# Performance work log

Measured on AMD Instinct MI355X. Metric: run time of the kernel, lower is better.

Reference implementation:

```python
import jax, jax.numpy as jnp
import numpy as np

B, T, C = 4, 2048, 2048
N_HEAD = 16
HEAD_DIM = C // N_HEAD


def setup_inputs() -> dict:
    key = jax.random.key(0)
    k1, k2, k3, k4, k5 = jax.random.split(key, 5)
    s = 1.0 / np.sqrt(C)
    return {
        "x": jax.random.normal(k1, (B, T, C), dtype=jnp.float32),
        "w_attn": jax.random.normal(k2, (C, 3 * C), dtype=jnp.float32) * s,
        "b_attn": jax.random.normal(k3, (3 * C,), dtype=jnp.float32) * 0.02,
        "w_proj": jax.random.normal(k4, (C, C), dtype=jnp.float32) * s,
        "b_proj": jax.random.normal(k5, (C,), dtype=jnp.float32) * 0.02,
    }


def reference(x, w_attn, b_attn, w_proj, b_proj):
    Bsz, Tlen, Cdim = x.shape
    # fused QKV projection
    qkv = x @ w_attn + b_attn  # [B,T,3C]
    q, k, v = jnp.split(qkv, 3, axis=-1)
    # [B,T,C] -> [B,H,T,D]
    def heads(t):
        return t.reshape(Bsz, Tlen, N_HEAD, HEAD_DIM).transpose(0, 2, 1, 3)
    q, k, v = heads(q), heads(k), heads(v)
    scale = 1.0 / np.sqrt(HEAD_DIM).astype(np.float32)
    att = jnp.einsum("bhqd,bhkd->bhqk", q, k) * scale  # [B,H,T,T]
    causal = jnp.tril(jnp.ones((Tlen, Tlen), dtype=bool))
    att = jnp.where(causal, att, -jnp.inf)
    att = jax.nn.softmax(att, axis=-1)
    y = jnp.einsum("bhqk,bhkd->bhqd", att, v)  # [B,H,T,D]
    y = y.transpose(0, 2, 1, 3).reshape(Bsz, Tlen, Cdim)
    return y @ w_proj + b_proj
```

## Files before the change

kernel.cpp:

```cpp
#include <hip/hip_runtime.h>

typedef __bf16 bf16x8 __attribute__((ext_vector_type(8)));
typedef __bf16 bf16x4 __attribute__((ext_vector_type(4)));
typedef float  f32x4  __attribute__((ext_vector_type(4)));
typedef float  f32x16 __attribute__((ext_vector_type(16)));
typedef unsigned u32x4 __attribute__((ext_vector_type(4)));

#define LOG2E 1.4426950408889634f

__device__ __forceinline__ void gload16(const void* g, void* l) {
  __builtin_amdgcn_global_load_lds((const __attribute__((address_space(1))) void*)g,
                                   (__attribute__((address_space(3))) void*)l, 16, 0, 0);
}

__device__ __forceinline__ unsigned pk(float lo, float hi) {
  unsigned short lu = __builtin_bit_cast(unsigned short, (__bf16)lo);
  unsigned short hu = __builtin_bit_cast(unsigned short, (__bf16)hi);
  return (unsigned)lu | ((unsigned)hu << 16);
}

__global__ __launch_bounds__(256) void cvt4(const float* __restrict__ in,
                                            __bf16* __restrict__ outp, int n4) {
  int i = blockIdx.x * blockDim.x + threadIdx.x;
  if (i < n4) {
    float4 v = ((const float4*)in)[i];
    bf16x4 o = { (__bf16)v.x, (__bf16)v.y, (__bf16)v.z, (__bf16)v.w };
    *(bf16x4*)(outp + (size_t)i * 4) = o;
  }
}

__global__ __launch_bounds__(256) void transcvt(const float* __restrict__ w,
                                                __bf16* __restrict__ wt,
                                                int K, int N) {
  __shared__ float tile[32][33];
  const int n0 = blockIdx.x * 32, k0 = blockIdx.y * 32;
  const int tx = threadIdx.x, ty = threadIdx.y;
#pragma unroll
  for (int i = 0; i < 4; ++i)
    tile[ty + i * 8][tx] = w[(size_t)(k0 + ty + i * 8) * N + n0 + tx];
  __syncthreads();
#pragma unroll
  for (int i = 0; i < 4; ++i)
    wt[(size_t)(n0 + ty + i * 8) * K + k0 + tx] = (__bf16)tile[tx][ty + i * 8];
}

template <int EPI, int NCOLS>
__global__ __launch_bounds__(512, 2)
void gemm_bt(const __bf16* __restrict__ A, const __bf16* __restrict__ Bt,
             const float* __restrict__ bias,
             __bf16* __restrict__ Qb, __bf16* __restrict__ Kb,
             __bf16* __restrict__ Vtb, float* __restrict__ Out) {
  constexpr int K = 2048;
  constexpr int NSTEP = K / 32;
  constexpr int NBX = NCOLS / 256;
  __shared__ __align__(16) __bf16 lds_[65536];
  __bf16* const As_ = lds_;
  __bf16* const Bs_ = lds_ + 32768;
  const int tid = threadIdx.x, lane = tid & 63, w = tid >> 6;
  const int wr = w >> 2, wc = w & 3;
  const int l15 = lane & 15, g = lane >> 4;

  const int nwg = (int)gridDim.x;
  const int flat = ((int)blockIdx.x & 7) * (nwg >> 3) + ((int)blockIdx.x >> 3);
  const int by = flat / NBX, bx = flat % NBX;

  const __bf16* Ab = A + (size_t)by * 256 * K;
  const __bf16* Bb = Bt + (size_t)bx * 256 * K;

  const int gsw = (((tid & 3) ^ ((tid >> 3) & 3)) * 8);
  const __bf16* srcA[2];
  const __bf16* srcB[2];
#pragma unroll
  for (int c = 0; c < 2; ++c) {
    const int idx = c * 512 + tid;
    const int row = idx >> 2;
    srcA[c] = Ab + (size_t)row * K + gsw;
    srcB[c] = Bb + (size_t)row * K + gsw;
  }
  const int ldst = tid * 8;

  const int csw = ((g ^ ((l15 >> 1) & 3)) * 8);

  f32x4 acc[8][4] = {};

#define ISSUE_A(jj) { const int s_ = ((jj) & 3) * 8192;                       \
    gload16(srcA[0] + (size_t)(jj) * 32, (void*)(As_ + s_ + ldst));           \
    gload16(srcA[1] + (size_t)(jj) * 32, (void*)(As_ + s_ + 4096 + ldst)); }
#define ISSUE_B(jj) { const int s_ = ((jj) & 3) * 8192;                       \
    gload16(srcB[0] + (size_t)(jj) * 32, (void*)(Bs_ + s_ + ldst));           \
    gload16(srcB[1] + (size_t)(jj) * 32, (void*)(Bs_ + s_ + 4096 + ldst)); }
#define VM8 asm volatile("s_waitcnt vmcnt(8)" ::: "memory")
#define VM4 asm volatile("s_waitcnt vmcnt(4)" ::: "memory")
#define VM0 asm volatile("s_waitcnt vmcnt(0)" ::: "memory")
#define VMN

#define KSTEP(j, ISS, VMW) {                                                  \
    const int rs = ((j) & 3) * 8192;                                          \
    bf16x8 av[8], bv[4];                                                      \
                           \
    _Pragma("unroll")                                                         \
    for (int i = 0; i < 4; ++i)                                               \
      bv[i] = *(const bf16x8*)(Bs_ + rs + (wc * 64 + i * 16 + l15) * 32 + csw); \
    _Pragma("unroll")                                                         \
    for (int i = 0; i < 4; ++i)                                               \
      av[i] = *(const bf16x8*)(As_ + rs + (wr * 128 + i * 16 + l15) * 32 + csw); \
    if (ISS) ISSUE_A((j) + 3);                                                \
    __builtin_amdgcn_s_barrier();                                             \
    __builtin_amdgcn_s_setprio(1);                                            \
    _Pragma("unroll")                                                         \
    for (int mi = 0; mi < 4; ++mi)                                            \
      _Pragma("unroll")                                                       \
      for (int ni = 0; ni < 4; ++ni)                                          \
        acc[mi][ni] = __builtin_amdgcn_mfma_f32_16x16x32_bf16(av[mi], bv[ni], \
                                                              acc[mi][ni], 0, 0, 0); \
    __builtin_amdgcn_s_setprio(0);                                            \
    __builtin_amdgcn_s_barrier();                                             \
            \
    _Pragma("unroll")                                                         \
    for (int i = 4; i < 8; ++i)                                               \
      av[i] = *(const bf16x8*)(As_ + rs + (wr * 128 + i * 16 + l15) * 32 + csw); \
    if (ISS) ISSUE_B((j) + 3);                                                \
    __builtin_amdgcn_s_barrier();                                             \
    __builtin_amdgcn_s_setprio(1);                                            \
    _Pragma("unroll")                                                         \
    for (int mi = 4; mi < 8; ++mi)                                            \
      _Pragma("unroll")                                                       \
      for (int ni = 0; ni < 4; ++ni)                                          \
        acc[mi][ni] = __builtin_amdgcn_mfma_f32_16x16x32_bf16(av[mi], bv[ni], \
                                                              acc[mi][ni], 0, 0, 0); \
    __builtin_amdgcn_s_setprio(0);                                            \
    VMW;                                                                      \
    __builtin_amdgcn_s_barrier();                                             \
  }

  ISSUE_A(0); ISSUE_B(0);
  ISSUE_A(1); ISSUE_B(1);
  ISSUE_A(2); ISSUE_B(2);
  VM8;
  __builtin_amdgcn_s_barrier();

  for (int j = 0; j < NSTEP - 3; ++j) KSTEP(j, true, VM8);
  KSTEP(NSTEP - 3, false, VM4);
  KSTEP(NSTEP - 2, false, VM0);
  KSTEP(NSTEP - 1, false, VMN);

#undef KSTEP
#undef ISSUE_A
#undef ISSUE_B

  const int r0 = by * 256 + wr * 128 + (g << 2);
  const int c0 = bx * 256 + wc * 64 + l15;
#pragma unroll
  for (int ni = 0; ni < 4; ++ni) {
    const int c = c0 + ni * 16;
    const float bvs = bias[c];
    if constexpr (EPI == 0) {
      const int sel = c >> 11, cc = c & 2047, h = cc >> 7, d = cc & 127;
#pragma unroll
      for (int mi = 0; mi < 8; ++mi) {
        const int r = r0 + mi * 16;
        const int bb = r >> 11, t = r & 2047;
        if (sel == 2) {
          bf16x4 pv;
#pragma unroll
          for (int j = 0; j < 4; ++j) pv[j] = (__bf16)(acc[mi][ni][j] + bvs);
          *(bf16x4*)(Vtb + ((size_t)(bb * 16 + h) * 128 + d) * 2048 + t) = pv;
        } else {
          __bf16* dst = (sel == 0 ? Qb : Kb) + ((size_t)(bb * 16 + h) * 2048 + t) * 128 + d;
          const float sc = (sel == 0) ? 0.08838834764831845f : 1.0f;
#pragma unroll
          for (int j = 0; j < 4; ++j)
            dst[(size_t)j * 128] = (__bf16)((acc[mi][ni][j] + bvs) * sc);
        }
      }
    } else {
#pragma unroll
      for (int mi = 0; mi < 8; ++mi) {
        const int r = r0 + mi * 16;
#pragma unroll
        for (int j = 0; j < 4; ++j)
          Out[(size_t)(r + j) * NCOLS + c] = acc[mi][ni][j] + bvs;
      }
    }
  }
}

__global__ __launch_bounds__(512, 2)
void attn_fwd(const __bf16* __restrict__ Qb, const __bf16* __restrict__ Kb,
              const __bf16* __restrict__ Vtb, __bf16* __restrict__ Yb) {
  __shared__ __align__(16) char lds[65536];
  const int tid = threadIdx.x;
  const int lane = tid & 63, w = tid >> 6;
  const int l31 = lane & 31, hi = lane >> 5;
  const int kx = (l31 & 7) << 4;

  const int G = (int)gridDim.x;
  for (int rr = 0;; ++rr) {
    const int pos = (rr & 1) ? (G - 1 - (int)blockIdx.x) : (int)blockIdx.x;
    const int item = rr * G + pos;
    if (item >= 512) break;
    const int qb = 7 - (item >> 6);
    const int bh = item & 63;
    const int bidx = bh >> 4, h = bh & 15;
    const int nt = (qb + 1) * 4;

    const __bf16* Qh = Qb + ((size_t)bh * 2048 + qb * 256) * 128;
    const __bf16* Kh = Kb + (size_t)bh * 2048 * 128;
    const __bf16* Vh = Vtb + (size_t)bh * 128 * 2048;

    bf16x8 qf[8];
    {
      const __bf16* qrow = Qh + (size_t)(w * 32 + l31) * 128 + hi * 8;
#pragma unroll
      for (int ds = 0; ds < 8; ++ds) qf[ds] = *(const bf16x8*)(qrow + ds * 16);
    }

    {
      uint4 kr[2], vr[2];
#pragma unroll
      for (int c = 0; c < 2; ++c) {
        const int idx = c * 512 + tid;
        kr[c] = *(const uint4*)(Kh + (size_t)(idx >> 4) * 128 + (idx & 15) * 8);
        vr[c] = *(const uint4*)(Vh + (size_t)(idx >> 3) * 2048 + (idx & 7) * 8);
      }
      __syncthreads();
      char* K0 = lds;
      char* V0 = lds + 16384;
#pragma unroll
      for (int c = 0; c < 2; ++c) {
        const int idx = c * 512 + tid;
        { const int row = idx >> 4, colB = (idx & 15) * 16;
          *(uint4*)(K0 + row * 256 + (colB ^ ((row & 7) << 4))) = kr[c]; }
        { const int row = idx >> 3, colB = (idx & 7) * 16;
          *(uint4*)(V0 + row * 128 + (colB ^ ((row & 7) << 4))) = vr[c]; }
      }
      __syncthreads();
    }

    f32x16 accO[4] = {};
    float mL = -3.0e38f, lsum = 0.f;
    const int qg  = qb * 256 + w * 32 + l31;
    const int qwb = qb * 256 + w * 32;

    for (int t = 0; t < nt; ++t) {
      const int kv0 = t * 64;
      char* Kc = lds + (t & 1) * 32768;
      char* Vc = Kc + 16384;
      const bool pf = (t + 1 < nt);
      uint4 kr[2], vr[2];
      if (pf) {
        const int kvn = kv0 + 64;
#pragma unroll
        for (int c = 0; c < 2; ++c) {
          const int idx = c * 512 + tid;
          kr[c] = *(const uint4*)(Kh + (size_t)(kvn + (idx >> 4)) * 128 + (idx & 15) * 8);
          vr[c] = *(const uint4*)(Vh + (size_t)(idx >> 3) * 2048 + kvn + (idx & 7) * 8);
        }
      }

      f32x16 s0 = {}, s1 = {};
      __builtin_amdgcn_s_setprio(1);
#pragma unroll
      for (int ds = 0; ds < 8; ++ds) {
        const int cb = (ds * 32 + hi * 16) ^ kx;
        bf16x8 k0 = *(const bf16x8*)(Kc + l31 * 256 + cb);
        bf16x8 k1 = *(const bf16x8*)(Kc + (32 + l31) * 256 + cb);
        s0 = __builtin_amdgcn_mfma_f32_32x32x16_bf16(k0, qf[ds], s0, 0, 0, 0);
        s1 = __builtin_amdgcn_mfma_f32_32x32x16_bf16(k1, qf[ds], s1, 0, 0, 0);
      }
      __builtin_amdgcn_s_setprio(0);

      f32x16 a0, a1;
#pragma unroll
      for (int r = 0; r < 16; ++r) { a0[r] = s0[r] * LOG2E; a1[r] = s1[r] * LOG2E; }
      if (kv0 + 63 > qwb) {
#pragma unroll
        for (int r = 0; r < 16; ++r) {
          const int kvr = kv0 + (r & 3) + 8 * (r >> 2) + 4 * hi;
          if (kvr > qg)      a0[r] = -1.0e38f;
          if (kvr + 32 > qg) a1[r] = -1.0e38f;
        }
      }

      float pm = a0[0];
#pragma unroll
      for (int r = 1; r < 16; ++r) pm = fmaxf(pm, a0[r]);
#pragma unroll
      for (int r = 0; r < 16; ++r) pm = fmaxf(pm, a1[r]);
      pm = fmaxf(pm, __shfl_xor(pm, 32, 64));

      if (!__all(pm - mL <= 11.5f)) {
        const float mn = fmaxf(mL, pm);
        const float corr = exp2f(mL - mn);
        mL = mn;
        lsum *= corr;
#pragma unroll
        for (int db = 0; db < 4; ++db)
#pragma unroll
          for (int r = 0; r < 16; ++r) accO[db][r] *= corr;
      }

      float p[32];
      float rs = 0.f;
#pragma unroll
      for (int r = 0; r < 16; ++r) { p[r] = exp2f(a0[r] - mL); rs += p[r]; }
#pragma unroll
      for (int r = 0; r < 16; ++r) { p[16 + r] = exp2f(a1[r] - mL); rs += p[16 + r]; }
      rs += __shfl_xor(rs, 32, 64);
      lsum += rs;

      bf16x8 pa[4];
#pragma unroll
      for (int f = 0; f < 2; ++f) {
        unsigned wv[8];
#pragma unroll
        for (int i = 0; i < 8; ++i)
          wv[i] = pk(p[f * 16 + 2 * i], p[f * 16 + 2 * i + 1]);
        const unsigned x0 = (unsigned)__shfl_xor((int)(hi ? wv[0] : wv[2]), 32, 64);
        const unsigned x1 = (unsigned)__shfl_xor((int)(hi ? wv[1] : wv[3]), 32, 64);
        const unsigned x2 = (unsigned)__shfl_xor((int)(hi ? wv[4] : wv[6]), 32, 64);
        const unsigned x3 = (unsigned)__shfl_xor((int)(hi ? wv[5] : wv[7]), 32, 64);
        u32x4 A, B;
        A[0] = hi ? x0 : wv[0];  A[1] = hi ? x1 : wv[1];
        A[2] = hi ? wv[2] : x0;  A[3] = hi ? wv[3] : x1;
        B[0] = hi ? x2 : wv[4];  B[1] = hi ? x3 : wv[5];
        B[2] = hi ? wv[6] : x2;  B[3] = hi ? wv[7] : x3;
        pa[f * 2 + 0] = __builtin_bit_cast(bf16x8, A);
        pa[f * 2 + 1] = __builtin_bit_cast(bf16x8, B);
      }

      __builtin_amdgcn_s_setprio(1);
#pragma unroll
      for (int ks = 0; ks < 4; ++ks) {
        const int cb = (ks * 32 + hi * 16) ^ kx;
#pragma unroll
        for (int db = 0; db < 4; ++db) {
          bf16x8 vf = *(const bf16x8*)(Vc + (db * 32 + l31) * 128 + cb);
          accO[db] = __builtin_amdgcn_mfma_f32_32x32x16_bf16(vf, pa[ks], accO[db], 0, 0, 0);
        }
      }
      __builtin_amdgcn_s_setprio(0);

      if (pf) {
        char* Kn = lds + ((t + 1) & 1) * 32768;
        char* Vn = Kn + 16384;
#pragma unroll
        for (int c = 0; c < 2; ++c) {
          const int idx = c * 512 + tid;
          { const int row = idx >> 4, colB = (idx & 15) * 16;
            *(uint4*)(Kn + row * 256 + (colB ^ ((row & 7) << 4))) = kr[c]; }
          { const int row = idx >> 3, colB = (idx & 7) * 16;
            *(uint4*)(Vn + row * 128 + (colB ^ ((row & 7) << 4))) = vr[c]; }
        }
      }
      __syncthreads();
    }

    const float rl = 1.0f / lsum;
    __bf16* Yw = Yb + ((size_t)bidx * 2048 + qg) * 2048 + h * 128;
#pragma unroll
    for (int db = 0; db < 4; ++db)
#pragma unroll
      for (int j = 0; j < 4; ++j) {
        bf16x4 o;
#pragma unroll
        for (int i = 0; i < 4; ++i) o[i] = (__bf16)(accO[db][4 * j + i] * rl);
        *(bf16x4*)(Yw + db * 32 + 8 * j + 4 * hi) = o;
      }
  }
}

extern "C" void kernel_launch(void* const* d_in, const int* in_sizes, int n_in,
                              void* d_out, int out_size, void* d_ws, size_t ws_size,
                              hipStream_t stream) {
  const float* x      = (const float*)d_in[0];
  const float* w_attn = (const float*)d_in[1];
  const float* b_attn = (const float*)d_in[2];
  const float* w_proj = (const float*)d_in[3];
  const float* b_proj = (const float*)d_in[4];
  float* out = (float*)d_out;

  __bf16* Qb  = (__bf16*)d_ws;
  __bf16* Kb  = Qb  + (size_t)16777216;
  __bf16* Vtb = Kb  + (size_t)16777216;
  __bf16* XYb = Vtb + (size_t)16777216;
  __bf16* Wt  = XYb + (size_t)16777216;

  cvt4<<<dim3(16384), dim3(256), 0, stream>>>(x, XYb, 4194304);
  transcvt<<<dim3(192, 64), dim3(32, 8), 0, stream>>>(w_attn, Wt, 2048, 6144);
  gemm_bt<0, 6144><<<dim3(768), dim3(512), 0, stream>>>(XYb, Wt, b_attn,
                                                        Qb, Kb, Vtb, nullptr);
  transcvt<<<dim3(64, 64), dim3(32, 8), 0, stream>>>(w_proj, Wt, 2048, 2048);
  attn_fwd<<<dim3(256), dim3(512), 0, stream>>>(Qb, Kb, Vtb, XYb);
  gemm_bt<1, 2048><<<dim3(256), dim3(512), 0, stream>>>(XYb, Wt, b_proj,
                                                        nullptr, nullptr, nullptr, out);
}
```

Before: 473.7 us.

## Software-pipeline LDS fragment loads across k-steps in GEMM main loop

Restructures the GEMM k-step so the LDS reads for A and B fragments are interleaved with MFMA groups, and the first A fragments plus all B fragments of the next stage are prefetched into double-buffered registers. Barriers drop from four per step to two, and the setprio hints are removed. The aim is to hide LDS latency behind MFMA work and cut synchronisation stalls. The cost is higher register pressure, and the loop is unrolled by two, which assumes NSTEP is even.

```diff
diff --git a/kernel.cpp b/kernel.cpp
--- a/kernel.cpp
+++ b/kernel.cpp
@@ -80,9 +80,13 @@
   const int ldst = tid * 8;
 
   const int csw = ((g ^ ((l15 >> 1) & 3)) * 8);
+  const int aoff = (wr * 128 + l15) * 32 + csw;
+  const int boff = (wc * 64 + l15) * 32 + csw;
 
   f32x4 acc[8][4] = {};
 
+#define LDA(rs, i) (*(const bf16x8*)(As_ + (rs) + aoff + (i) * 512))
+#define LDB(rs, i) (*(const bf16x8*)(Bs_ + (rs) + boff + (i) * 512))
 #define ISSUE_A(jj) { const int s_ = ((jj) & 3) * 8192;                       \
     gload16(srcA[0] + (size_t)(jj) * 32, (void*)(As_ + s_ + ldst));           \
     gload16(srcA[1] + (size_t)(jj) * 32, (void*)(As_ + s_ + 4096 + ldst)); }
@@ -93,60 +97,63 @@
 #define VM4 asm volatile("s_waitcnt vmcnt(4)" ::: "memory")
 #define VM0 asm volatile("s_waitcnt vmcnt(0)" ::: "memory")
 #define VMN
-
-#define KSTEP(j, ISS, VMW) {                                                  \
-    const int rs = ((j) & 3) * 8192;                                          \
-    bf16x8 av[8], bv[4];                                                      \
-                           \
-    _Pragma("unroll")                                                         \
-    for (int i = 0; i < 4; ++i)                                               \
-      bv[i] = *(const bf16x8*)(Bs_ + rs + (wc * 64 + i * 16 + l15) * 32 + csw); \
-    _Pragma("unroll")                                                         \
-    for (int i = 0; i < 4; ++i)                                               \
-      av[i] = *(const bf16x8*)(As_ + rs + (wr * 128 + i * 16 + l15) * 32 + csw); \
+#define MFMA8(p0, p1, bq, m0, m1)                                             \
+  _Pragma("unroll")                                                           \
+  for (int ni = 0; ni < 4; ++ni) {                                            \
+    acc[m0][ni] = __builtin_amdgcn_mfma_f32_16x16x32_bf16(p0, bq[ni],         \
+                                                          acc[m0][ni], 0,0,0);\
+    acc[m1][ni] = __builtin_amdgcn_mfma_f32_16x16x32_bf16(p1, bq[ni],         \
+                                                          acc[m1][ni], 0,0,0);\
+  }
+
+#define KSTEP(j, ISS, VMW, RB, avC, avN, bvC, bvN) {                          \
+    const int rs_ = ((j) & 3) * 8192;                                         \
+    const int rn_ = (((j) + 1) & 3) * 8192;                                   \
+    bf16x8 a2 = LDA(rs_, 2), a3 = LDA(rs_, 3);                                \
+    MFMA8(avC[0], avC[1], bvC, 0, 1);                                         \
+    bf16x8 a4 = LDA(rs_, 4), a5 = LDA(rs_, 5);                                \
+    MFMA8(a2, a3, bvC, 2, 3);                                                 \
     if (ISS) ISSUE_A((j) + 3);                                                \
-    __builtin_amdgcn_s_barrier();                                             \
-    __builtin_amdgcn_s_setprio(1);                                            \
-    _Pragma("unroll")                                                         \
-    for (int mi = 0; mi < 4; ++mi)                                            \
-      _Pragma("unroll")                                                       \
-      for (int ni = 0; ni < 4; ++ni)                                          \
-        acc[mi][ni] = __builtin_amdgcn_mfma_f32_16x16x32_bf16(av[mi], bv[ni], \
-                                                              acc[mi][ni], 0, 0, 0); \
-    __builtin_amdgcn_s_setprio(0);                                            \
-    __builtin_amdgcn_s_barrier();                                             \
-            \
-    _Pragma("unroll")                                                         \
-    for (int i = 4; i < 8; ++i)                                               \
-      av[i] = *(const bf16x8*)(As_ + rs + (wr * 128 + i * 16 + l15) * 32 + csw); \
+    bf16x8 a6 = LDA(rs_, 6), a7 = LDA(rs_, 7);                                \
+    MFMA8(a4, a5, bvC, 4, 5);                                                 \
     if (ISS) ISSUE_B((j) + 3);                                                \
-    __builtin_amdgcn_s_barrier();                                             \
-    __builtin_amdgcn_s_setprio(1);                                            \
-    _Pragma("unroll")                                                         \
-    for (int mi = 4; mi < 8; ++mi)                                            \
-      _Pragma("unroll")                                                       \
-      for (int ni = 0; ni < 4; ++ni)                                          \
-        acc[mi][ni] = __builtin_amdgcn_mfma_f32_16x16x32_bf16(av[mi], bv[ni], \
-                                                              acc[mi][ni], 0, 0, 0); \
-    __builtin_amdgcn_s_setprio(0);                                            \
     VMW;                                                                      \
     __builtin_amdgcn_s_barrier();                                             \
-  }
+    if (RB) {                                                                 \
+      avN[0] = LDA(rn_, 0); avN[1] = LDA(rn_, 1);                             \
+      bvN[0] = LDB(rn_, 0); bvN[1] = LDB(rn_, 1);                             \
+      bvN[2] = LDB(rn_, 2); bvN[3] = LDB(rn_, 3);                             \
+    }                                                                         \
+    MFMA8(a6, a7, bvC, 6, 7);                                                 \
+    __builtin_amdgcn_s_barrier();                                             \
+  }
+
+  bf16x8 avX[2], avY[2], bvX[4], bvY[4];
 
   ISSUE_A(0); ISSUE_B(0);
   ISSUE_A(1); ISSUE_B(1);
   ISSUE_A(2); ISSUE_B(2);
   VM8;
   __builtin_amdgcn_s_barrier();
-
-  for (int j = 0; j < NSTEP - 3; ++j) KSTEP(j, true, VM8);
-  KSTEP(NSTEP - 3, false, VM4);
-  KSTEP(NSTEP - 2, false, VM0);
-  KSTEP(NSTEP - 1, false, VMN);
+  avX[0] = LDA(0, 0); avX[1] = LDA(0, 1);
+  bvX[0] = LDB(0, 0); bvX[1] = LDB(0, 1);
+  bvX[2] = LDB(0, 2); bvX[3] = LDB(0, 3);
+
+  for (int j = 0; j < NSTEP - 4; j += 2) {
+    KSTEP(j,     true, VM8, true, avX, avY, bvX, bvY);
+    KSTEP(j + 1, true, VM8, true, avY, avX, bvY, bvX);
+  }
+  KSTEP(NSTEP - 4, true,  VM8, true,  avX, avY, bvX, bvY);
+  KSTEP(NSTEP - 3, false, VM4, true,  avY, avX, bvY, bvX);
+  KSTEP(NSTEP - 2, false, VM0, true,  avX, avY, bvX, bvY);
+  KSTEP(NSTEP - 1, false, VMN, false, avY, avX, bvY, bvX);
 
 #undef KSTEP
+#undef MFMA8
 #undef ISSUE_A
 #undef ISSUE_B
+#undef LDA
+#undef LDB
 
   const int r0 = by * 256 + wr * 128 + (g << 2);
   const int c0 = bx * 256 + wc * 64 + l15;
```

Result: no change. 472.7 us (-0.2%).
